# Kernel tuning notes

Measured on AMD Instinct MI355X. Metric: run time of the kernel, lower is better.

Reference implementation:

```python
import jax, jax.numpy as jnp
import numpy as np
import math

D_MODEL = 1024
NUM_HEADS = 16
D_HEAD = D_MODEL // NUM_HEADS


def setup_inputs() -> dict:
    key = jax.random.key(0)
    k1, k2, k3, k4, k5 = jax.random.split(key, 5)
    scale = 1.0 / math.sqrt(D_MODEL)
    x = jax.random.normal(k1, (4, 2048, D_MODEL), dtype=jnp.float32)
    W_qkv = jax.random.normal(k2, (D_MODEL, 3 * D_MODEL), dtype=jnp.float32) * scale
    b_qkv = jax.random.normal(k3, (3 * D_MODEL,), dtype=jnp.float32) * 0.02
    W_o = jax.random.normal(k4, (D_MODEL, D_MODEL), dtype=jnp.float32) * scale
    b_o = jax.random.normal(k5, (D_MODEL,), dtype=jnp.float32) * 0.02
    return {"x": x, "W_qkv": W_qkv, "b_qkv": b_qkv, "W_o": W_o, "b_o": b_o}


def reference(x, W_qkv, b_qkv, W_o, b_o):
    B, C, D = x.shape
    H, Dh = NUM_HEADS, D_HEAD
    qkv = x @ W_qkv + b_qkv                       # [B, C, 3D]
    qkv = qkv.reshape(B, C, 3, H, Dh).transpose(2, 0, 3, 1, 4)  # [3, B, H, C, Dh]
    Q, K, V = qkv[0], qkv[1], qkv[2]
    scores = jnp.einsum('bhqd,bhkd->bhqk', Q, K) / math.sqrt(Dh)  # [B, H, C, C]
    causal = jnp.tril(jnp.ones((C, C), dtype=bool))
    scores = jnp.where(causal, scores, -jnp.inf)
    weights = jax.nn.softmax(scores, axis=-1)
    attn = jnp.einsum('bhqk,bhkd->bhqd', weights, V)              # [B, H, C, Dh]
    attn = attn.transpose(0, 2, 1, 3).reshape(B, C, D)
    return attn @ W_o + b_o
```

## Files before the change

### kernel.cpp

```cpp
#include <hip/hip_runtime.h>
#include <hip/hip_bf16.h>
#include <stdint.h>


typedef __attribute__((ext_vector_type(8))) short short8;
typedef __attribute__((ext_vector_type(4))) short short4v;
typedef __attribute__((ext_vector_type(4))) float f32x4;

#define AS1 __attribute__((address_space(1)))
#define AS3 __attribute__((address_space(3)))

static __device__ __forceinline__ short f2bf(float f) {
  union { float f; uint32_t u; } v; v.f = f;
  uint32_t r = v.u + 0x7fffu + ((v.u >> 16) & 1u);
  return (short)(r >> 16);
}

static __device__ __forceinline__ short f2bfh(float f) {
  __hip_bfloat16 h = __float2bfloat16(f);
  return *reinterpret_cast<short*>(&h);
}

static __device__ __forceinline__ void gload_lds16(const void* g, void* l) {
  __builtin_amdgcn_global_load_lds((const AS1 void*)g, (AS3 void*)l, 16, 0, 0);
}

#define MFMA16(a, b, c) __builtin_amdgcn_mfma_f32_16x16x32_bf16((a), (b), (c), 0, 0, 0)

__global__ __launch_bounds__(256) void k_cvt_x(const float* __restrict__ x,
                                               short* __restrict__ xb) {
  long i = ((long)blockIdx.x * 256 + threadIdx.x) * 4;
  const float4 v = *(const float4*)(x + i);
  short4v o;
  o[0] = f2bf(v.x); o[1] = f2bf(v.y); o[2] = f2bf(v.z); o[3] = f2bf(v.w);
  *(short4v*)(xb + i) = o;
}

__global__ __launch_bounds__(256) void k_transpose_bf(const float* __restrict__ W,
                                                      short* __restrict__ Wt,
                                                      int K, int N) {
  __shared__ float t[64][65];
  const int nb = blockIdx.x * 64, kb = blockIdx.y * 64;
  const int tid = threadIdx.x;
#pragma unroll
  for (int i = 0; i < 16; ++i) {
    int idx = i * 256 + tid; int r = idx >> 6, c = idx & 63;
    t[r][c] = W[(long)(kb + r) * N + nb + c];
  }
  __syncthreads();
#pragma unroll
  for (int i = 0; i < 16; ++i) {
    int idx = i * 256 + tid; int r = idx >> 6, c = idx & 63;
    Wt[(long)(nb + r) * K + kb + c] = f2bf(t[c][r]);
  }
}

template <int EPI>
__global__ __launch_bounds__(512, 2)
void k_gemm(const short* __restrict__ A, const short* __restrict__ Bt,
            const float* __restrict__ bias, float* __restrict__ Cf,
            short* __restrict__ q_ws, short* __restrict__ k_ws, short* __restrict__ vt_ws,
            int M, int N, int K) {
  __shared__ __align__(16) short a_sh[2][128 * 64];
  __shared__ __align__(16) short b_sh[2][256 * 64];
  const int tid = threadIdx.x;
  const int lane = tid & 63, wid = tid >> 6;
  const int l15 = lane & 15, lg = lane >> 4;
  const int s7 = l15 & 7;
  const int wgm = wid >> 2, wgn = wid & 3;
  const int m0 = blockIdx.y * 128, n0 = blockIdx.x * 256;

  f32x4 acc[2][4][2] = {};

  const int srow = tid >> 3, sgr = tid & 7;

#define STAGE_A(buf, kb, j)                                                          \
  {                                                                                  \
    int row = (j) * 64 + srow;                                                       \
    gload_lds16(A + (long)(m0 + row) * K + (kb) + ((sgr ^ (row & 7)) << 3),          \
                &a_sh[buf][((j) * 512 + tid) * 8]);                                  \
  }
#define STAGE_B(buf, kb, j)                                                          \
  {                                                                                  \
    int row = (j) * 64 + srow;                                                       \
    gload_lds16(Bt + (long)(n0 + row) * K + (kb) + ((sgr ^ (row & 7)) << 3),         \
                &b_sh[buf][((j) * 512 + tid) * 8]);                                  \
  }

  STAGE_A(0, 0, 0); STAGE_A(0, 0, 1);
  STAGE_B(0, 0, 0); STAGE_B(0, 0, 1); STAGE_B(0, 0, 2); STAGE_B(0, 0, 3);
  asm volatile("s_waitcnt vmcnt(2)" ::: "memory");
  __builtin_amdgcn_sched_barrier(0);
  __builtin_amdgcn_s_barrier();

  const int nt = K >> 6;
  int cur = 0;
  for (int t = 0; t < nt; ++t) {
    const int kb2 = (t + 1) << 6;
    const bool pre = (t + 1 < nt);

    short8 af[4][2], bf[2][2];
#pragma unroll
    for (int mi = 0; mi < 4; ++mi)
#pragma unroll
      for (int kk = 0; kk < 2; ++kk) {
        const int row = (wgm * 4 + mi) * 16 + l15;
        af[mi][kk] = *(const short8*)(&a_sh[cur][row * 64 + (((kk * 4 + lg) ^ s7) << 3)]);
      }
#pragma unroll
    for (int ni = 0; ni < 2; ++ni)
#pragma unroll
      for (int kk = 0; kk < 2; ++kk) {
        const int row = (wgn * 2 + ni) * 16 + l15;
        bf[ni][kk] = *(const short8*)(&b_sh[cur][row * 64 + (((kk * 4 + lg) ^ s7) << 3)]);
      }
    if (pre) { STAGE_A(cur ^ 1, kb2, 0); STAGE_A(cur ^ 1, kb2, 1); STAGE_B(cur ^ 1, kb2, 0); }
    __builtin_amdgcn_s_barrier();
    __builtin_amdgcn_s_setprio(1);
#pragma unroll
    for (int mi = 0; mi < 4; ++mi)
#pragma unroll
      for (int ni = 0; ni < 2; ++ni)
#pragma unroll
        for (int kk = 0; kk < 2; ++kk)
          acc[0][mi][ni] = MFMA16(af[mi][kk], bf[ni][kk], acc[0][mi][ni]);
    __builtin_amdgcn_s_setprio(0);
    if (pre) asm volatile("s_waitcnt vmcnt(3)" ::: "memory");
    else     asm volatile("s_waitcnt vmcnt(0)" ::: "memory");
    __builtin_amdgcn_sched_barrier(0);
    __builtin_amdgcn_s_barrier();

    short8 bg[2][2];
#pragma unroll
    for (int ni = 0; ni < 2; ++ni)
#pragma unroll
      for (int kk = 0; kk < 2; ++kk) {
        const int row = 128 + (wgn * 2 + ni) * 16 + l15;
        bg[ni][kk] = *(const short8*)(&b_sh[cur][row * 64 + (((kk * 4 + lg) ^ s7) << 3)]);
      }
    if (pre) { STAGE_B(cur ^ 1, kb2, 1); STAGE_B(cur ^ 1, kb2, 2); STAGE_B(cur ^ 1, kb2, 3); }
    __builtin_amdgcn_s_barrier();
    __builtin_amdgcn_s_setprio(1);
#pragma unroll
    for (int mi = 0; mi < 4; ++mi)
#pragma unroll
      for (int ni = 0; ni < 2; ++ni)
#pragma unroll
        for (int kk = 0; kk < 2; ++kk)
          acc[1][mi][ni] = MFMA16(af[mi][kk], bg[ni][kk], acc[1][mi][ni]);
    __builtin_amdgcn_s_setprio(0);
    if (pre) {
      asm volatile("s_waitcnt vmcnt(2)" ::: "memory");
      __builtin_amdgcn_sched_barrier(0);
    }
    __builtin_amdgcn_s_barrier();
    cur ^= 1;
  }
#undef STAGE_A
#undef STAGE_B

#pragma unroll
  for (int h = 0; h < 2; ++h) {
#pragma unroll
    for (int mi = 0; mi < 4; ++mi) {
#pragma unroll
      for (int ni = 0; ni < 2; ++ni) {
        const int n = n0 + h * 128 + (wgn * 2 + ni) * 16 + l15;
        const int mb = m0 + (wgm * 4 + mi) * 16 + lg * 4;
        if (EPI == 1) {
#pragma unroll
          for (int r = 0; r < 4; ++r)
            Cf[(long)(mb + r) * N + n] = acc[h][mi][ni][r] + bias[n];
        } else {
          const int which = n >> 10;
          const int hh = (n >> 6) & 15, d = n & 63;
          const int b = mb >> 11, c = mb & 2047;
          const int bh = b * 16 + hh;
          const float bi = bias[n];
          if (which == 2) {
            short4v o;
#pragma unroll
            for (int r = 0; r < 4; ++r) o[r] = f2bf(acc[h][mi][ni][r] + bi);
            *(short4v*)(vt_ws + ((long)bh * 64 + d) * 2048 + c) = o;
          } else if (which == 0) {
#pragma unroll
            for (int r = 0; r < 4; ++r)
              q_ws[((long)bh * 2048 + c + r) * 64 + d] = f2bf((acc[h][mi][ni][r] + bi) * 0.18033688011f);
          } else {
#pragma unroll
            for (int r = 0; r < 4; ++r)
              k_ws[((long)bh * 2048 + c + r) * 64 + d] = f2bf(acc[h][mi][ni][r] + bi);
          }
        }
      }
    }
  }
}

__global__ __launch_bounds__(128)
void k_attn(const short* __restrict__ q_ws, const short* __restrict__ k_ws,
            const short* __restrict__ vt_ws, short* __restrict__ attn_out) {
  __shared__ __align__(16) short k_sh[2][64 * 64];
  __shared__ __align__(16) short v_sh[2][64 * 64];

  const int tid = threadIdx.x;
  const int lane = tid & 63, wid = tid >> 6;
  const int l15 = lane & 15, lg = lane >> 4;
  const int bh = blockIdx.x;
  const int qt = (int)gridDim.y - 1 - (int)blockIdx.y;
  const int b = bh >> 4, h = bh & 15;
  const int qwA = qt * 64 + wid * 16;
  const int qwB = qwA + 32;
  const int qA = qwA + l15, qB = qwB + l15;
  const int nt = qt + 1;

  const short* qrowA = q_ws + ((long)bh * 2048 + qA) * 64;
  const short* qrowB = q_ws + ((long)bh * 2048 + qB) * 64;
  const short8 qfA0 = *(const short8*)(qrowA + lg * 8);
  const short8 qfA1 = *(const short8*)(qrowA + 32 + lg * 8);
  const short8 qfB0 = *(const short8*)(qrowB + lg * 8);
  const short8 qfB1 = *(const short8*)(qrowB + 32 + lg * 8);

  const int s7 = l15 & 7;
  const int koff0 = ((lg ^ s7) << 4);
  const int koff1 = (((4 + lg) ^ s7) << 4);
  const int vsub = (lg & 1) * 8, vg = lg >> 1;
  int voff[4];
#pragma unroll
  for (int m2 = 0; m2 < 4; ++m2)
    voff[m2] = (((2 * m2 + vg) ^ s7) << 4) | vsub;

  f32x4 accA[4] = {}, accB[4] = {};
  float lA = 0.f, lB = 0.f;

  const int srow = tid >> 3, sg = tid & 7;

#define STAGE(buf, kv)                                                              \
  {                                                                                 \
    _Pragma("unroll")                                                               \
    for (int i = 0; i < 4; ++i) {                                                   \
      int row = i * 16 + srow;                                                      \
      int gl = sg ^ (row & 7);                                                      \
      gload_lds16(k_ws + ((long)bh * 2048 + (kv) + row) * 64 + gl * 8,              \
                  &k_sh[buf][(i * 128 + tid) * 8]);                                 \
      gload_lds16(vt_ws + ((long)bh * 64 + row) * 2048 + (kv) + gl * 8,             \
                  &v_sh[buf][(i * 128 + tid) * 8]);                                 \
    }                                                                               \
  }

  STAGE(0, 0);
  asm volatile("s_waitcnt vmcnt(0)" ::: "memory");
  __syncthreads();

  int cur = 0;
  for (int t = 0; t < nt; ++t) {
    const int kv0 = t * 64;
    if (t + 1 < nt) STAGE(cur ^ 1, kv0 + 64);

    const char* ksh = (const char*)k_sh[cur];
    const char* vsh = (const char*)v_sh[cur];

    f32x4 stA[4], stB[4];
    __builtin_amdgcn_s_setprio(1);
#pragma unroll
    for (int j = 0; j < 4; ++j) {
      const char* kr = ksh + (j * 16 + l15) * 128;
      short8 kf0 = *(const short8*)(kr + koff0);
      short8 kf1 = *(const short8*)(kr + koff1);
      f32x4 zA = {};
      zA = MFMA16(kf0, qfA0, zA);
      zA = MFMA16(kf1, qfA1, zA);
      stA[j] = zA;
      f32x4 zB = {};
      zB = MFMA16(kf0, qfB0, zB);
      zB = MFMA16(kf1, qfB1, zB);
      stB[j] = zB;
    }
    __builtin_amdgcn_s_setprio(0);

    if (t == nt - 1) {
#pragma unroll
      for (int j = 0; j < 4; ++j) {
        int kvr = kv0 + j * 16 + lg * 4;
#pragma unroll
        for (int r = 0; r < 4; ++r) {
          if (kvr + r > qA) stA[j][r] = -1e30f;
          if (kvr + r > qB) stB[j][r] = -1e30f;
        }
      }
    }

    short8 pA0, pA1, pB0, pB1;
    {
      float ps = 0.f;
#pragma unroll
      for (int j = 0; j < 4; ++j)
#pragma unroll
        for (int r = 0; r < 4; ++r) {
          float e = __builtin_amdgcn_exp2f(stA[j][r]);
          stA[j][r] = e;
          ps += e;
        }
      lA += ps;
#pragma unroll
      for (int r = 0; r < 4; ++r) {
        pA0[r]     = f2bfh(stA[0][r]);
        pA0[4 + r] = f2bfh(stA[1][r]);
        pA1[r]     = f2bfh(stA[2][r]);
        pA1[4 + r] = f2bfh(stA[3][r]);
      }
    }
    {
      float ps = 0.f;
#pragma unroll
      for (int j = 0; j < 4; ++j)
#pragma unroll
        for (int r = 0; r < 4; ++r) {
          float e = __builtin_amdgcn_exp2f(stB[j][r]);
          stB[j][r] = e;
          ps += e;
        }
      lB += ps;
#pragma unroll
      for (int r = 0; r < 4; ++r) {
        pB0[r]     = f2bfh(stB[0][r]);
        pB0[4 + r] = f2bfh(stB[1][r]);
        pB1[r]     = f2bfh(stB[2][r]);
        pB1[4 + r] = f2bfh(stB[3][r]);
      }
    }

    __builtin_amdgcn_s_setprio(1);
#pragma unroll
    for (int dt = 0; dt < 4; ++dt) {
      const char* vr = vsh + (dt * 16 + l15) * 128;
      union { short8 s8; short4v s4[2]; } vf1, vf2;
      vf1.s4[0] = *(const short4v*)(vr + voff[0]);
      vf1.s4[1] = *(const short4v*)(vr + voff[1]);
      vf2.s4[0] = *(const short4v*)(vr + voff[2]);
      vf2.s4[1] = *(const short4v*)(vr + voff[3]);
      accA[dt] = MFMA16(vf1.s8, pA0, accA[dt]);
      accA[dt] = MFMA16(vf2.s8, pA1, accA[dt]);
      accB[dt] = MFMA16(vf1.s8, pB0, accB[dt]);
      accB[dt] = MFMA16(vf2.s8, pB1, accB[dt]);
    }
    __builtin_amdgcn_s_setprio(0);

    asm volatile("s_waitcnt vmcnt(0)" ::: "memory");
    __syncthreads();
    cur ^= 1;
  }
#undef STAGE

  {
    float lt = lA;
    lt += __shfl_xor(lt, 16);
    lt += __shfl_xor(lt, 32);
    const float inv = 1.0f / lt;
    short* obase = attn_out + ((long)b * 2048 + qA) * 1024 + h * 64;
#pragma unroll
    for (int dt = 0; dt < 4; ++dt) {
      short4v o;
#pragma unroll
      for (int r = 0; r < 4; ++r) o[r] = f2bfh(accA[dt][r] * inv);
      *(short4v*)(obase + dt * 16 + lg * 4) = o;
    }
  }
  {
    float lt = lB;
    lt += __shfl_xor(lt, 16);
    lt += __shfl_xor(lt, 32);
    const float inv = 1.0f / lt;
    short* obase = attn_out + ((long)b * 2048 + qB) * 1024 + h * 64;
#pragma unroll
    for (int dt = 0; dt < 4; ++dt) {
      short4v o;
#pragma unroll
      for (int r = 0; r < 4; ++r) o[r] = f2bfh(accB[dt][r] * inv);
      *(short4v*)(obase + dt * 16 + lg * 4) = o;
    }
  }
}

extern "C" void kernel_launch(void* const* d_in, const int* in_sizes, int n_in,
                              void* d_out, int out_size, void* d_ws, size_t ws_size,
                              hipStream_t stream) {
  const float* x     = (const float*)d_in[0];
  const float* W_qkv = (const float*)d_in[1];
  const float* b_qkv = (const float*)d_in[2];
  const float* W_o   = (const float*)d_in[3];
  const float* b_o   = (const float*)d_in[4];
  float* out = (float*)d_out;

  char* ws = (char*)d_ws;
  short* x_bf   = (short*)(ws);
  short* wqkv_t = (short*)(ws + 16777216);
  short* wo_t   = (short*)(ws + 23068672);
  short* q_ws   = (short*)(ws + 25165824);
  short* k_ws   = (short*)(ws + 41943040);
  short* vt_ws  = (short*)(ws + 58720256);

  k_cvt_x<<<dim3(8192), dim3(256), 0, stream>>>(x, x_bf);
  k_transpose_bf<<<dim3(48, 16), dim3(256), 0, stream>>>(W_qkv, wqkv_t, 1024, 3072);
  k_transpose_bf<<<dim3(16, 16), dim3(256), 0, stream>>>(W_o, wo_t, 1024, 1024);
  k_gemm<0><<<dim3(12, 64), dim3(512), 0, stream>>>(x_bf, wqkv_t, b_qkv, nullptr,
                                                    q_ws, k_ws, vt_ws, 8192, 3072, 1024);
  k_attn<<<dim3(64, 32), dim3(128), 0, stream>>>(q_ws, k_ws, vt_ws, x_bf);
  k_gemm<1><<<dim3(4, 64), dim3(512), 0, stream>>>(x_bf, wo_t, b_o, out,
                                                   nullptr, nullptr, nullptr, 8192, 1024, 1024);
}
```

Before: 170.9 us.

## Triple-buffer LDS in GEMM kernel and prefetch two K-tiles ahead

After: 162.4 us. 1.05x faster.

```diff
diff --git a/kernel.cpp b/kernel.cpp
--- a/kernel.cpp
+++ b/kernel.cpp
@@ -61,8 +61,8 @@
             const float* __restrict__ bias, float* __restrict__ Cf,
             short* __restrict__ q_ws, short* __restrict__ k_ws, short* __restrict__ vt_ws,
             int M, int N, int K) {
-  __shared__ __align__(16) short a_sh[2][128 * 64];
-  __shared__ __align__(16) short b_sh[2][256 * 64];
+  __shared__ __align__(16) short a_sh[3][128 * 64];
+  __shared__ __align__(16) short b_sh[3][256 * 64];
   const int tid = threadIdx.x;
   const int lane = tid & 63, wid = tid >> 6;
   const int l15 = lane & 15, lg = lane >> 4;
@@ -86,18 +86,25 @@
     gload_lds16(Bt + (long)(n0 + row) * K + (kb) + ((sgr ^ (row & 7)) << 3),         \
                 &b_sh[buf][((j) * 512 + tid) * 8]);                                  \
   }
-
-  STAGE_A(0, 0, 0); STAGE_A(0, 0, 1);
-  STAGE_B(0, 0, 0); STAGE_B(0, 0, 1); STAGE_B(0, 0, 2); STAGE_B(0, 0, 3);
-  asm volatile("s_waitcnt vmcnt(2)" ::: "memory");
+#define STAGE6(buf, kb)                                                              \
+  {                                                                                  \
+    STAGE_A(buf, kb, 0); STAGE_A(buf, kb, 1);                                        \
+    STAGE_B(buf, kb, 0); STAGE_B(buf, kb, 1); STAGE_B(buf, kb, 2); STAGE_B(buf, kb, 3); \
+  }
+
+  STAGE6(0, 0);
+  STAGE6(1, 64);
+  asm volatile("s_waitcnt vmcnt(6)" ::: "memory");
   __builtin_amdgcn_sched_barrier(0);
   __builtin_amdgcn_s_barrier();
+  __builtin_amdgcn_sched_barrier(0);
 
   const int nt = K >> 6;
-  int cur = 0;
+  int rd = 0;
   for (int t = 0; t < nt; ++t) {
-    const int kb2 = (t + 1) << 6;
-    const bool pre = (t + 1 < nt);
+    const int wr = (rd >= 1) ? rd - 1 : rd + 2;
+    const int kb2 = (t + 2) << 6;
+    const bool pre = (t + 2 < nt);
 
     short8 af[4][2], bf[2][2];
 #pragma unroll
@@ -105,17 +112,16 @@
 #pragma unroll
       for (int kk = 0; kk < 2; ++kk) {
         const int row = (wgm * 4 + mi) * 16 + l15;
-        af[mi][kk] = *(const short8*)(&a_sh[cur][row * 64 + (((kk * 4 + lg) ^ s7) << 3)]);
+        af[mi][kk] = *(const short8*)(&a_sh[rd][row * 64 + (((kk * 4 + lg) ^ s7) << 3)]);
       }
 #pragma unroll
     for (int ni = 0; ni < 2; ++ni)
 #pragma unroll
       for (int kk = 0; kk < 2; ++kk) {
         const int row = (wgn * 2 + ni) * 16 + l15;
-        bf[ni][kk] = *(const short8*)(&b_sh[cur][row * 64 + (((kk * 4 + lg) ^ s7) << 3)]);
-      }
-    if (pre) { STAGE_A(cur ^ 1, kb2, 0); STAGE_A(cur ^ 1, kb2, 1); STAGE_B(cur ^ 1, kb2, 0); }
-    __builtin_amdgcn_s_barrier();
+        bf[ni][kk] = *(const short8*)(&b_sh[rd][row * 64 + (((kk * 4 + lg) ^ s7) << 3)]);
+      }
+    if (pre) { STAGE_A(wr, kb2, 0); STAGE_A(wr, kb2, 1); STAGE_B(wr, kb2, 0); }
     __builtin_amdgcn_s_setprio(1);
 #pragma unroll
     for (int mi = 0; mi < 4; ++mi)
@@ -125,39 +131,36 @@
         for (int kk = 0; kk < 2; ++kk)
           acc[0][mi][ni] = MFMA16(af[mi][kk], bf[ni][kk], acc[0][mi][ni]);
     __builtin_amdgcn_s_setprio(0);
-    if (pre) asm volatile("s_waitcnt vmcnt(3)" ::: "memory");
+
+    short8 bg[2][2];
+#pragma unroll
+    for (int ni = 0; ni < 2; ++ni)
+#pragma unroll
+      for (int kk = 0; kk < 2; ++kk) {
+        const int row = 128 + (wgn * 2 + ni) * 16 + l15;
+        bg[ni][kk] = *(const short8*)(&b_sh[rd][row * 64 + (((kk * 4 + lg) ^ s7) << 3)]);
+      }
+    if (pre) { STAGE_B(wr, kb2, 1); STAGE_B(wr, kb2, 2); STAGE_B(wr, kb2, 3); }
+    __builtin_amdgcn_s_setprio(1);
+#pragma unroll
+    for (int mi = 0; mi < 4; ++mi)
+#pragma unroll
+      for (int ni = 0; ni < 2; ++ni)
+#pragma unroll
+        for (int kk = 0; kk < 2; ++kk)
+          acc[1][mi][ni] = MFMA16(af[mi][kk], bg[ni][kk], acc[1][mi][ni]);
+    __builtin_amdgcn_s_setprio(0);
+
+    if (pre) asm volatile("s_waitcnt vmcnt(6)" ::: "memory");
     else     asm volatile("s_waitcnt vmcnt(0)" ::: "memory");
     __builtin_amdgcn_sched_barrier(0);
     __builtin_amdgcn_s_barrier();
-
-    short8 bg[2][2];
-#pragma unroll
-    for (int ni = 0; ni < 2; ++ni)
-#pragma unroll
-      for (int kk = 0; kk < 2; ++kk) {
-        const int row = 128 + (wgn * 2 + ni) * 16 + l15;
-        bg[ni][kk] = *(const short8*)(&b_sh[cur][row * 64 + (((kk * 4 + lg) ^ s7) << 3)]);
-      }
-    if (pre) { STAGE_B(cur ^ 1, kb2, 1); STAGE_B(cur ^ 1, kb2, 2); STAGE_B(cur ^ 1, kb2, 3); }
-    __builtin_amdgcn_s_barrier();
-    __builtin_amdgcn_s_setprio(1);
-#pragma unroll
-    for (int mi = 0; mi < 4; ++mi)
-#pragma unroll
-      for (int ni = 0; ni < 2; ++ni)
-#pragma unroll
-        for (int kk = 0; kk < 2; ++kk)
-          acc[1][mi][ni] = MFMA16(af[mi][kk], bg[ni][kk], acc[1][mi][ni]);
-    __builtin_amdgcn_s_setprio(0);
-    if (pre) {
-      asm volatile("s_waitcnt vmcnt(2)" ::: "memory");
-      __builtin_amdgcn_sched_barrier(0);
-    }
-    __builtin_amdgcn_s_barrier();
-    cur ^= 1;
+    __builtin_amdgcn_sched_barrier(0);
+    rd = (rd == 2) ? 0 : rd + 1;
   }
 #undef STAGE_A
 #undef STAGE_B
+#undef STAGE6
 
 #pragma unroll
   for (int h = 0; h < 2; ++h) {
```
